# Performance work log

Hardware: AMD Instinct MI355X
Metric: run time of the kernel (lower is better)

The kernel has to match this reference:

```python
import jax, jax.numpy as jnp
import numpy as np

B, S, D, H, DFF = 8, 1024, 1024, 16, 4096
DK = D // H
EPS = 1e-6
NEG = -1e9


def setup_inputs() -> dict:
    key = jax.random.key(0)
    ks = jax.random.split(key, 8)
    x = jax.random.normal(ks[0], (B, S, D), dtype=jnp.float32)
    mask = jnp.ones((B, 1, 1, S), dtype=jnp.int32)
    s = 0.02
    wq = jax.random.normal(ks[1], (D, D), jnp.float32) * s
    wk = jax.random.normal(ks[2], (D, D), jnp.float32) * s
    wv = jax.random.normal(ks[3], (D, D), jnp.float32) * s
    wo = jax.random.normal(ks[4], (D, D), jnp.float32) * s
    bq = jnp.zeros((D,), jnp.float32); bk = jnp.zeros((D,), jnp.float32)
    bv = jnp.zeros((D,), jnp.float32); bo = jnp.zeros((D,), jnp.float32)
    w1 = jax.random.normal(ks[5], (D, DFF), jnp.float32) * s
    b1 = jnp.zeros((DFF,), jnp.float32)
    w2 = jax.random.normal(ks[6], (DFF, D), jnp.float32) * s
    b2 = jnp.zeros((D,), jnp.float32)
    g1 = jnp.array(1.0, jnp.float32); be1 = jnp.array(0.0, jnp.float32)
    g2 = jnp.array(1.0, jnp.float32); be2 = jnp.array(0.0, jnp.float32)
    return dict(x=x, mask=mask, wq=wq, bq=bq, wk=wk, bk=bk, wv=wv, bv=bv,
                wo=wo, bo=bo, w1=w1, b1=b1, w2=w2, b2=b2,
                g1=g1, be1=be1, g2=g2, be2=be2)


def layer_norm(x, gamma, beta):
    # repo quirk: unbiased std (ddof=1), scalar gamma/beta, divide by (std+eps)
    mean = jnp.mean(x, axis=-1, keepdims=True)
    std = jnp.std(x, axis=-1, keepdims=True, ddof=1)
    return gamma * (x - mean) / (std + EPS) + beta


def mha(x, mask, wq, bq, wk, bk, wv, bv, wo, bo):
    q = (x @ wq + bq).reshape(B, S, H, DK).transpose(0, 2, 1, 3)  # bhsd
    k = (x @ wk + bk).reshape(B, S, H, DK).transpose(0, 2, 1, 3)
    v = (x @ wv + bv).reshape(B, S, H, DK).transpose(0, 2, 1, 3)
    scores = jnp.einsum('bhqd,bhkd->bhqk', q, k) / jnp.sqrt(jnp.float32(DK))
    scores = jnp.where(mask == 0, NEG, scores)
    attn = jax.nn.softmax(scores, axis=-1)
    out = jnp.einsum('bhqk,bhkd->bhqd', attn, v)
    out = out.transpose(0, 2, 1, 3).reshape(B, S, D)
    return out @ wo + bo


def reference(x, mask, wq, bq, wk, bk, wv, bv, wo, bo, w1, b1, w2, b2, g1, be1, g2, be2):
    # pre-LN residual: x + sublayer(norm(x)); dropout inert at eval
    x = x + mha(layer_norm(x, g1, be1), mask, wq, bq, wk, bk, wv, bv, wo, bo)
    h = layer_norm(x, g2, be2)
    x = x + (jax.nn.relu(h @ w1 + b1) @ w2 + b2)
    return x
```

## Files before the change

kernel.cpp:

```cpp
#include <hip/hip_runtime.h>
#include <math.h>

typedef __bf16 bf16;
typedef float f32x4 __attribute__((ext_vector_type(4)));
typedef bf16 bf16x8 __attribute__((ext_vector_type(8)));
typedef bf16 bf16x4 __attribute__((ext_vector_type(4)));

#define DEV __device__ __forceinline__

constexpr int Ss = 1024, Dd = 1024;
constexpr float EPSf = 1e-6f;
constexpr float SM_SCALE = 0.125f * 1.4426950408889634f;

DEV void gl_lds16(const void* g, void* l) {
  __builtin_amdgcn_global_load_lds(
      (const __attribute__((address_space(1))) void*)g,
      (__attribute__((address_space(3))) void*)l, 16, 0, 0);
}

__global__ __launch_bounds__(256) void transpose6_k(
    const float* __restrict__ i0, const float* __restrict__ i1,
    const float* __restrict__ i2, const float* __restrict__ i3,
    const float* __restrict__ i4, const float* __restrict__ i5,
    bf16* __restrict__ o0, bf16* __restrict__ o1, bf16* __restrict__ o2,
    bf16* __restrict__ o3, bf16* __restrict__ o4, bf16* __restrict__ o5) {
  __shared__ float t[64 * 65];
  const int bi = blockIdx.x;
  const float* in;
  bf16* out;
  int R, C, local, sh;
  if (bi < 1024) {
    const int j = bi >> 8;
    local = bi & 255; R = 1024; C = 1024; sh = 4;
    in = (j == 0) ? i0 : (j == 1) ? i1 : (j == 2) ? i2 : i3;
    out = (j == 0) ? o0 : (j == 1) ? o1 : (j == 2) ? o2 : o3;
  } else if (bi < 2048) {
    local = bi - 1024; R = 1024; C = 4096; sh = 6; in = i4; out = o4;
  } else {
    local = bi - 2048; R = 4096; C = 1024; sh = 4; in = i5; out = o5;
  }
  const int nx = 1 << sh;
  const int bx = local & (nx - 1), by = local >> sh;
  const int tid = threadIdx.x;
  const int tx = tid & 63, ty = tid >> 6;
  const int r0 = by * 64, c0 = bx * 64;
#pragma unroll
  for (int i = 0; i < 16; i++) {
    int r = ty + i * 4;
    t[r * 65 + tx] = in[(size_t)(r0 + r) * C + c0 + tx];
  }
  __syncthreads();
#pragma unroll
  for (int i = 0; i < 16; i++) {
    int r = ty + i * 4;
    out[(size_t)(c0 + r) * R + r0 + tx] = (bf16)t[tx * 65 + r];
  }
}

__global__ __launch_bounds__(256) void ln_kernel(
    const float* __restrict__ in, bf16* __restrict__ out,
    const float* __restrict__ gp, const float* __restrict__ bp) {
  const int row = blockIdx.x;
  const int tid = threadIdx.x;
  float v[4];
  const float* p = in + (size_t)row * Dd + tid * 4;
#pragma unroll
  for (int i = 0; i < 4; i++) v[i] = p[i];
  float s = v[0] + v[1] + v[2] + v[3];
  float s2 = v[0] * v[0] + v[1] * v[1] + v[2] * v[2] + v[3] * v[3];
#pragma unroll
  for (int m = 1; m < 64; m <<= 1) {
    s += __shfl_xor(s, m, 64);
    s2 += __shfl_xor(s2, m, 64);
  }
  __shared__ float ls[4], ls2[4];
  if ((tid & 63) == 0) {
    ls[tid >> 6] = s;
    ls2[tid >> 6] = s2;
  }
  __syncthreads();
  s = ls[0] + ls[1] + ls[2] + ls[3];
  s2 = ls2[0] + ls2[1] + ls2[2] + ls2[3];
  float mean = s * (1.0f / Dd);
  float var = (s2 - (float)Dd * mean * mean) * (1.0f / (Dd - 1));
  var = fmaxf(var, 0.0f);
  float g = gp[0], be = bp[0];
  float rs = g / (sqrtf(var) + EPSf);
  bf16* q = out + (size_t)row * Dd + tid * 4;
#pragma unroll
  for (int i = 0; i < 4; i++) q[i] = (bf16)((v[i] - mean) * rs + be);
}

template <int EPI, int BK>
__global__ __launch_bounds__(256) void gemm_bt(
    const bf16* __restrict__ A, const bf16* __restrict__ Bt,
    const float* __restrict__ bias, const float* __restrict__ bias2,
    const float* __restrict__ bias3, const float* __restrict__ resid,
    bf16* __restrict__ vtb, void* __restrict__ Cout, int M, int N, int K,
    int sa, int sb) {
  __shared__ __attribute__((aligned(16))) char smem[2 * 128 * BK * 2];
  bf16* As = (bf16*)smem;
  bf16* Bs = (bf16*)(smem + 128 * BK * 2);
  constexpr int CPR = BK / 8;
  constexpr int RPJ = 256 / CPR;
  constexpr int NJ = BK / 16;
  const int tid = threadIdx.x;
  const int ln = tid & 63;
  const int wv = tid >> 6;
  const int wm = wv >> 1, wn = wv & 1;
  const int quad = ln >> 4, l16 = ln & 15;
  const int l7 = l16 & 7;
  const int m0 = blockIdx.y * 128, n0 = blockIdx.x * 128;

  f32x4 acc[4][4];
#pragma unroll
  for (int i = 0; i < 4; i++)
#pragma unroll
    for (int j = 0; j < 4; j++) acc[i][j] = {0.f, 0.f, 0.f, 0.f};

  const int sr = tid / CPR;
  const int sc = (tid & (CPR - 1)) ^ (sr & 7);
  const size_t abase = (size_t)(m0 + sr) * sa + sc * 8;
  const size_t bbase = (size_t)(n0 + sr) * sb + sc * 8;

  for (int k0 = 0; k0 < K; k0 += BK) {
#pragma unroll
    for (int j = 0; j < NJ; j++) {
      gl_lds16(A + abase + (size_t)(j * RPJ) * sa + k0,
               (char*)As + j * 4096 + wv * 1024);
      gl_lds16(Bt + bbase + (size_t)(j * RPJ) * sb + k0,
               (char*)Bs + j * 4096 + wv * 1024);
    }
    __syncthreads();
#pragma unroll
    for (int kh = 0; kh < BK / 32; kh++) {
      bf16x8 af[4], bfr[4];
#pragma unroll
      for (int mi = 0; mi < 4; mi++)
        af[mi] = *(const bf16x8*)&As[(wm * 64 + mi * 16 + l16) * BK +
                                     ((kh * 4 + quad) ^ l7) * 8];
#pragma unroll
      for (int ni = 0; ni < 4; ni++)
        bfr[ni] = *(const bf16x8*)&Bs[(wn * 64 + ni * 16 + l16) * BK +
                                      ((kh * 4 + quad) ^ l7) * 8];
#pragma unroll
      for (int mi = 0; mi < 4; mi++)
#pragma unroll
        for (int ni = 0; ni < 4; ni++)
          acc[mi][ni] = __builtin_amdgcn_mfma_f32_16x16x32_bf16(
              af[mi], bfr[ni], acc[mi][ni], 0, 0, 0);
    }
    __syncthreads();
  }

  if constexpr (EPI == 4) {
    if (n0 < 2048) {
#pragma unroll
      for (int mi = 0; mi < 4; mi++) {
        const int m = m0 + wm * 64 + mi * 16 + quad * 4;
#pragma unroll
        for (int ni = 0; ni < 4; ni++) {
          const int n = n0 + wn * 64 + ni * 16 + l16;
          const float bvl = (n < 1024) ? bias[n] : bias2[n - 1024];
#pragma unroll
          for (int r = 0; r < 4; r++)
            ((bf16*)Cout)[(size_t)(m + r) * N + n] =
                (bf16)(acc[mi][ni][r] + bvl);
        }
      }
    } else {
      bf16* T = (bf16*)smem;
#pragma unroll
      for (int mi = 0; mi < 4; mi++) {
        const int ml = wm * 64 + mi * 16 + quad * 4;
        const int c = ml >> 3, hf = (ml >> 2) & 1;
#pragma unroll
        for (int ni = 0; ni < 4; ni++) {
          const int nl = wn * 64 + ni * 16 + l16;
          const float bvl = bias3[(n0 - 2048) + nl];
          bf16x4 tv;
#pragma unroll
          for (int r = 0; r < 4; r++) tv[r] = (bf16)(acc[mi][ni][r] + bvl);
          *(bf16x4*)&T[nl * 128 + ((c ^ (nl & 15)) << 3) + (hf << 2)] = tv;
        }
      }
      __syncthreads();
      const size_t vbase =
          ((size_t)(m0 >> 10) * 1024 + (n0 - 2048)) * Ss + (m0 & 1023);
#pragma unroll
      for (int p = 0; p < 8; p++) {
        const int row = p * 16 + (tid >> 4);
        const int k = tid & 15;
        bf16x8 vv = *(const bf16x8*)&T[row * 128 + ((k ^ (row & 15)) << 3)];
        *(bf16x8*)&vtb[vbase + (size_t)row * Ss + k * 8] = vv;
      }
    }
  } else {
#pragma unroll
    for (int mi = 0; mi < 4; mi++) {
      const int m = m0 + wm * 64 + mi * 16 + quad * 4;
#pragma unroll
      for (int ni = 0; ni < 4; ni++) {
        const int n = n0 + wn * 64 + ni * 16 + l16;
        float bvl = 0.0f;
        if constexpr (EPI != 3) bvl = bias[n];
#pragma unroll
        for (int r = 0; r < 4; r++) {
          float val = acc[mi][ni][r] + bvl;
          const size_t idx = (size_t)(m + r) * N + n;
          if constexpr (EPI == 1) {
            ((float*)Cout)[idx] = val + resid[idx];
          } else if constexpr (EPI == 2) {
            ((bf16*)Cout)[idx] = (bf16)fmaxf(val, 0.0f);
          } else {
            ((float*)Cout)[idx] = val + resid[idx];
          }
        }
      }
    }
  }
}

__global__ __launch_bounds__(256) void attn_k(
    const bf16* __restrict__ qkv, const bf16* __restrict__ vt,
    const int* __restrict__ mask, bf16* __restrict__ ctx) {
  __shared__ __attribute__((aligned(16))) char smem[36864];
  bf16* Qs = (bf16*)smem;
  bf16* Ks = (bf16*)(smem + 16384);
  bf16* Vs = (bf16*)(smem + 24576);
  float* Fm = (float*)(smem + 32768);
  bf16* Ps = Qs;
  const int tid = threadIdx.x;
  const int ln = tid & 63, w = tid >> 6;
  const int quad = ln >> 4, l16 = ln & 15;
  const int l7 = l16 & 7;
  const int bh = blockIdx.y;
  const int b = bh >> 4, h = bh & 15;
  const int q0 = blockIdx.x * 128;
  const int sr = tid >> 3;
  const int sc = (tid & 7) ^ (sr & 7);

  {
#pragma unroll
    for (int j = 0; j < 4; j++) {
      const size_t ga =
          (size_t)(b * Ss + q0 + j * 32 + sr) * 3072 + h * 64 + sc * 8;
      gl_lds16(qkv + ga, (char*)Qs + j * 4096 + w * 1024);
    }
  }
  {
    const int4 mv = *(const int4*)&mask[b * Ss + tid * 4];
    const float ninf = -__builtin_inff();
    Fm[tid * 4 + 0] = mv.x ? 0.0f : ninf;
    Fm[tid * 4 + 1] = mv.y ? 0.0f : ninf;
    Fm[tid * 4 + 2] = mv.z ? 0.0f : ninf;
    Fm[tid * 4 + 3] = mv.w ? 0.0f : ninf;
  }
  __syncthreads();
  bf16x8 aq[2][2];
#pragma unroll
  for (int qi = 0; qi < 2; qi++)
#pragma unroll
    for (int c = 0; c < 2; c++)
      aq[qi][c] = *(const bf16x8*)&Qs[(w * 32 + qi * 16 + l16) * 64 +
                                      ((c * 4 + quad) ^ l7) * 8];

  bf16x8 ONE;
#pragma unroll
  for (int i = 0; i < 8; i++) ONE[i] = (bf16)1.0f;

  f32x4 o[2][4];
#pragma unroll
  for (int qi = 0; qi < 2; qi++)
#pragma unroll
    for (int i = 0; i < 4; i++) o[qi][i] = {0.f, 0.f, 0.f, 0.f};
  f32x4 osum[2] = {{0.f, 0.f, 0.f, 0.f}, {0.f, 0.f, 0.f, 0.f}};

  for (int kk0 = 0; kk0 < Ss; kk0 += 64) {
    {
#pragma unroll
      for (int j = 0; j < 2; j++) {
        const size_t ga = (size_t)(b * Ss + kk0 + j * 32 + sr) * 3072 + 1024 +
                          h * 64 + sc * 8;
        gl_lds16(qkv + ga, (char*)Ks + j * 4096 + w * 1024);
        const size_t gv = (size_t)(bh * 64 + j * 32 + sr) * Ss + kk0 + sc * 8;
        gl_lds16(vt + gv, (char*)Vs + j * 4096 + w * 1024);
      }
    }
    __syncthreads();

    f32x4 st[2][4];
#pragma unroll
    for (int nt = 0; nt < 4; nt++) {
      bf16x8 bk0 = *(const bf16x8*)&Ks[(nt * 16 + l16) * 64 + (quad ^ l7) * 8];
      bf16x8 bk1 =
          *(const bf16x8*)&Ks[(nt * 16 + l16) * 64 + ((4 + quad) ^ l7) * 8];
#pragma unroll
      for (int qi = 0; qi < 2; qi++) {
        f32x4 s = {0.f, 0.f, 0.f, 0.f};
        s = __builtin_amdgcn_mfma_f32_16x16x32_bf16(aq[qi][0], bk0, s, 0, 0, 0);
        s = __builtin_amdgcn_mfma_f32_16x16x32_bf16(aq[qi][1], bk1, s, 0, 0, 0);
        st[qi][nt] = s;
      }
    }
    float fmv[4];
#pragma unroll
    for (int nt = 0; nt < 4; nt++) fmv[nt] = Fm[kk0 + nt * 16 + l16];
#pragma unroll
    for (int qi = 0; qi < 2; qi++)
#pragma unroll
      for (int nt = 0; nt < 4; nt++)
#pragma unroll
        for (int r = 0; r < 4; r++)
          st[qi][nt][r] = exp2f(fmaf(st[qi][nt][r], SM_SCALE, fmv[nt]));
#pragma unroll
    for (int qi = 0; qi < 2; qi++)
#pragma unroll
      for (int nt = 0; nt < 4; nt++) {
        const int ch = nt * 2 + (l16 >> 3);
#pragma unroll
        for (int r = 0; r < 4; r++) {
          const int pr = qi * 16 + quad * 4 + r;
          Ps[w * 2048 + pr * 64 + (ch ^ (pr & 7)) * 8 + l7] =
              (bf16)st[qi][nt][r];
        }
      }
#pragma unroll
    for (int kh = 0; kh < 2; kh++) {
      bf16x8 bv[4];
#pragma unroll
      for (int dt = 0; dt < 4; dt++)
        bv[dt] = *(const bf16x8*)&Vs[(dt * 16 + l16) * 64 +
                                     ((kh * 4 + quad) ^ l7) * 8];
#pragma unroll
      for (int qi = 0; qi < 2; qi++) {
        bf16x8 ap = *(const bf16x8*)&Ps[w * 2048 + (qi * 16 + l16) * 64 +
                                        ((kh * 4 + quad) ^ l7) * 8];
#pragma unroll
        for (int dt = 0; dt < 4; dt++)
          o[qi][dt] =
              __builtin_amdgcn_mfma_f32_16x16x32_bf16(ap, bv[dt], o[qi][dt],
                                                      0, 0, 0);
        osum[qi] =
            __builtin_amdgcn_mfma_f32_16x16x32_bf16(ap, ONE, osum[qi], 0, 0, 0);
      }
    }
    __syncthreads();
  }
#pragma unroll
  for (int qi = 0; qi < 2; qi++) {
    const float inv0 = 1.0f / osum[qi][0], inv1 = 1.0f / osum[qi][1];
    const float inv2 = 1.0f / osum[qi][2], inv3 = 1.0f / osum[qi][3];
#pragma unroll
    for (int dt = 0; dt < 4; dt++) {
      const size_t base =
          (size_t)(b * Ss + q0 + w * 32 + qi * 16 + quad * 4) * Dd + h * 64 +
          dt * 16 + l16;
      ctx[base] = (bf16)(o[qi][dt][0] * inv0);
      ctx[base + Dd] = (bf16)(o[qi][dt][1] * inv1);
      ctx[base + 2 * Dd] = (bf16)(o[qi][dt][2] * inv2);
      ctx[base + 3 * Dd] = (bf16)(o[qi][dt][3] * inv3);
    }
  }
}

extern "C" void kernel_launch(void* const* d_in, const int* in_sizes, int n_in,
                              void* d_out, int out_size, void* d_ws,
                              size_t ws_size, hipStream_t stream) {
  (void)in_sizes; (void)n_in; (void)out_size;
  const float* x = (const float*)d_in[0];
  const int* mask = (const int*)d_in[1];
  const float* wq = (const float*)d_in[2];
  const float* bq = (const float*)d_in[3];
  const float* wk = (const float*)d_in[4];
  const float* bk = (const float*)d_in[5];
  const float* wvw = (const float*)d_in[6];
  const float* bv = (const float*)d_in[7];
  const float* wo = (const float*)d_in[8];
  const float* bo = (const float*)d_in[9];
  const float* w1 = (const float*)d_in[10];
  const float* b1 = (const float*)d_in[11];
  const float* w2 = (const float*)d_in[12];
  const float* b2 = (const float*)d_in[13];
  const float* g1 = (const float*)d_in[14];
  const float* be1 = (const float*)d_in[15];
  const float* g2 = (const float*)d_in[16];
  const float* be2 = (const float*)d_in[17];
  float* out = (float*)d_out;

  char* ws = (char*)d_ws;
  const size_t MB = 1024 * 1024;
  bf16* w1T = (bf16*)(ws + 0 * MB);
  bf16* w2T = (bf16*)(ws + 8 * MB);
  bf16* wqkvT = (bf16*)(ws + 16 * MB);
  bf16* woT = (bf16*)(ws + 22 * MB);
  bf16* lnb = (bf16*)(ws + 24 * MB);
  bf16* qkv = (bf16*)(ws + 40 * MB);
  bf16* vtb = (bf16*)(ws + 88 * MB);
  float* x1 = (float*)(ws + 40 * MB);
  bf16* ctx = lnb;

  dim3 blk(256);
  transpose6_k<<<3072, blk, 0, stream>>>(
      wq, wk, wvw, wo, w1, w2, wqkvT, wqkvT + (size_t)1024 * 1024,
      wqkvT + (size_t)2048 * 1024, woT, w1T, w2T);
  ln_kernel<<<8192, blk, 0, stream>>>(x, lnb, g1, be1);
  gemm_bt<4, 64><<<dim3(24, 64), blk, 0, stream>>>(
      lnb, wqkvT, bq, bk, bv, nullptr, vtb, qkv, 8192, 3072, 1024, 1024, 1024);
  attn_k<<<dim3(8, 128), blk, 0, stream>>>(qkv, vtb, mask, ctx);
  gemm_bt<1, 128><<<dim3(8, 64), blk, 0, stream>>>(
      ctx, woT, bo, nullptr, nullptr, x, nullptr, x1, 8192, 1024, 1024, 1024,
      1024);
  ln_kernel<<<8192, blk, 0, stream>>>(x1, lnb, g2, be2);

  if (ws_size >= 136 * MB) {
    bf16* mid = (bf16*)(ws + 72 * MB);
    gemm_bt<2, 64><<<dim3(32, 64), blk, 0, stream>>>(
        lnb, w1T, b1, nullptr, nullptr, nullptr, nullptr, mid, 8192, 4096,
        1024, 1024, 1024);
    gemm_bt<1, 128><<<dim3(8, 64), blk, 0, stream>>>(
        mid, w2T, b2, nullptr, nullptr, x1, nullptr, out, 8192, 1024, 4096,
        4096, 4096);
  } else {
    bf16* mid = (bf16*)(ws + 72 * MB);
    gemm_bt<2, 64><<<dim3(16, 64), blk, 0, stream>>>(
        lnb, w1T, b1, nullptr, nullptr, nullptr, nullptr, mid, 8192, 2048,
        1024, 1024, 1024);
    gemm_bt<1, 128><<<dim3(8, 64), blk, 0, stream>>>(
        mid, w2T, b2, nullptr, nullptr, x1, nullptr, out, 8192, 1024, 2048,
        2048, 4096);
    gemm_bt<2, 64><<<dim3(16, 64), blk, 0, stream>>>(
        lnb, w1T + (size_t)2048 * 1024, b1 + 2048, nullptr, nullptr, nullptr,
        nullptr, mid, 8192, 2048, 1024, 1024, 1024);
    gemm_bt<3, 128><<<dim3(8, 64), blk, 0, stream>>>(
        mid, w2T + 2048, nullptr, nullptr, nullptr, out, nullptr, out, 8192,
        1024, 2048, 2048, 4096);
  }
}
```

Baseline: 494.6 us.

## Load K/V tiles directly from global into registers, drop LDS staging and barriers

The attention kernel stops staging K and V tiles in shared memory. Each wave now loads its MFMA B operands for K and V straight from global memory into registers, which removes both per-iteration __syncthreads and shrinks LDS use. The cost is that all four waves load the same K/V data independently, quadrupling global/L2 traffic, and nothing is prefetched ahead of the loop. Lower LDS use may allow more blocks per CU.

New measurement: 542.8 us. 1.1x slower.

```diff
diff --git a/kernel.cpp b/kernel.cpp
--- a/kernel.cpp
+++ b/kernel.cpp
@@ -224,11 +224,9 @@
 __global__ __launch_bounds__(256) void attn_k(
     const bf16* __restrict__ qkv, const bf16* __restrict__ vt,
     const int* __restrict__ mask, bf16* __restrict__ ctx) {
-  __shared__ __attribute__((aligned(16))) char smem[36864];
+  __shared__ __attribute__((aligned(16))) char smem[20480];
   bf16* Qs = (bf16*)smem;
-  bf16* Ks = (bf16*)(smem + 16384);
-  bf16* Vs = (bf16*)(smem + 24576);
-  float* Fm = (float*)(smem + 32768);
+  float* Fm = (float*)(smem + 16384);
   bf16* Ps = Qs;
   const int tid = threadIdx.x;
   const int ln = tid & 63, w = tid >> 6;
@@ -264,6 +262,7 @@
     for (int c = 0; c < 2; c++)
       aq[qi][c] = *(const bf16x8*)&Qs[(w * 32 + qi * 16 + l16) * 64 +
                                       ((c * 4 + quad) ^ l7) * 8];
+  __syncthreads();
 
   bf16x8 ONE;
 #pragma unroll
@@ -276,33 +275,38 @@
     for (int i = 0; i < 4; i++) o[qi][i] = {0.f, 0.f, 0.f, 0.f};
   f32x4 osum[2] = {{0.f, 0.f, 0.f, 0.f}, {0.f, 0.f, 0.f, 0.f}};
 
+  const bf16* kb0 =
+      qkv + (size_t)(b * Ss + l16) * 3072 + 1024 + h * 64 + quad * 8;
+  const bf16* vb0 = vt + (size_t)(bh * 64 + l16) * Ss + quad * 8;
+
   for (int kk0 = 0; kk0 < Ss; kk0 += 64) {
-    {
-#pragma unroll
-      for (int j = 0; j < 2; j++) {
-        const size_t ga = (size_t)(b * Ss + kk0 + j * 32 + sr) * 3072 + 1024 +
-                          h * 64 + sc * 8;
-        gl_lds16(qkv + ga, (char*)Ks + j * 4096 + w * 1024);
-        const size_t gv = (size_t)(bh * 64 + j * 32 + sr) * Ss + kk0 + sc * 8;
-        gl_lds16(vt + gv, (char*)Vs + j * 4096 + w * 1024);
-      }
-    }
-    __syncthreads();
+    bf16x8 bv[2][4];
+#pragma unroll
+    for (int kh = 0; kh < 2; kh++)
+#pragma unroll
+      for (int dt = 0; dt < 4; dt++)
+        bv[kh][dt] =
+            *(const bf16x8*)(vb0 + (size_t)(dt * 16) * Ss + kk0 + kh * 32);
+    bf16x8 bk[4][2];
+#pragma unroll
+    for (int nt = 0; nt < 4; nt++)
+#pragma unroll
+      for (int c = 0; c < 2; c++)
+        bk[nt][c] =
+            *(const bf16x8*)(kb0 + (size_t)(kk0 + nt * 16) * 3072 + c * 32);
 
     f32x4 st[2][4];
 #pragma unroll
-    for (int nt = 0; nt < 4; nt++) {
-      bf16x8 bk0 = *(const bf16x8*)&Ks[(nt * 16 + l16) * 64 + (quad ^ l7) * 8];
-      bf16x8 bk1 =
-          *(const bf16x8*)&Ks[(nt * 16 + l16) * 64 + ((4 + quad) ^ l7) * 8];
+    for (int nt = 0; nt < 4; nt++)
 #pragma unroll
       for (int qi = 0; qi < 2; qi++) {
         f32x4 s = {0.f, 0.f, 0.f, 0.f};
-        s = __builtin_amdgcn_mfma_f32_16x16x32_bf16(aq[qi][0], bk0, s, 0, 0, 0);
-        s = __builtin_amdgcn_mfma_f32_16x16x32_bf16(aq[qi][1], bk1, s, 0, 0, 0);
+        s = __builtin_amdgcn_mfma_f32_16x16x32_bf16(aq[qi][0], bk[nt][0], s,
+                                                    0, 0, 0);
+        s = __builtin_amdgcn_mfma_f32_16x16x32_bf16(aq[qi][1], bk[nt][1], s,
+                                                    0, 0, 0);
         st[qi][nt] = s;
       }
-    }
     float fmv[4];
 #pragma unroll
     for (int nt = 0; nt < 4; nt++) fmv[nt] = Fm[kk0 + nt * 16 + l16];
@@ -327,25 +331,18 @@
       }
 #pragma unroll
     for (int kh = 0; kh < 2; kh++) {
-      bf16x8 bv[4];
-#pragma unroll
-      for (int dt = 0; dt < 4; dt++)
-        bv[dt] = *(const bf16x8*)&Vs[(dt * 16 + l16) * 64 +
-                                     ((kh * 4 + quad) ^ l7) * 8];
 #pragma unroll
       for (int qi = 0; qi < 2; qi++) {
         bf16x8 ap = *(const bf16x8*)&Ps[w * 2048 + (qi * 16 + l16) * 64 +
                                         ((kh * 4 + quad) ^ l7) * 8];
 #pragma unroll
         for (int dt = 0; dt < 4; dt++)
-          o[qi][dt] =
-              __builtin_amdgcn_mfma_f32_16x16x32_bf16(ap, bv[dt], o[qi][dt],
-                                                      0, 0, 0);
+          o[qi][dt] = __builtin_amdgcn_mfma_f32_16x16x32_bf16(
+              ap, bv[kh][dt], o[qi][dt], 0, 0, 0);
         osum[qi] =
             __builtin_amdgcn_mfma_f32_16x16x32_bf16(ap, ONE, osum[qi], 0, 0, 0);
       }
     }
-    __syncthreads();
   }
 #pragma unroll
   for (int qi = 0; qi < 2; qi++) {
```
